# Kernel tuning notes

Measured on AMD Instinct MI355X. Metric: run time of the kernel, lower is better.

## Reference

```python
import jax, jax.numpy as jnp
import numpy as np

B, T, N = 32, 1024, 256
D = 1024          # latent_dim
TD = 768          # text_latent_dim
H = 16            # num_head
C = D // H        # head dim
TE = 2048         # time_embed_dim
EPS = 1e-5


def layer_norm(x, g, b):
    mu = jnp.mean(x, axis=-1, keepdims=True)
    var = jnp.var(x, axis=-1, keepdims=True)
    return (x - mu) * jax.lax.rsqrt(var + EPS) * g + b


def setup_inputs() -> dict:
    key = jax.random.key(0)
    ks = jax.random.split(key, 16)
    s_d = 1.0 / np.sqrt(D)
    s_td = 1.0 / np.sqrt(TD)
    s_te = 1.0 / np.sqrt(TE)
    return {
        "x": jax.random.normal(ks[0], (B, T, D), jnp.float32),
        "xf": jax.random.normal(ks[1], (B, N, TD), jnp.float32),
        "emb": jax.random.normal(ks[2], (B, TE), jnp.float32),
        "norm_g": jnp.ones((D,), jnp.float32),
        "norm_b": jnp.zeros((D,), jnp.float32),
        "tnorm_g": jnp.ones((TD,), jnp.float32),
        "tnorm_b": jnp.zeros((TD,), jnp.float32),
        "Wq": jax.random.normal(ks[3], (D, D), jnp.float32) * s_d,
        "bq": jnp.zeros((D,), jnp.float32),
        "Wk": jax.random.normal(ks[4], (TD, D), jnp.float32) * s_td,
        "bk": jnp.zeros((D,), jnp.float32),
        "Wv": jax.random.normal(ks[5], (TD, D), jnp.float32) * s_td,
        "bv": jnp.zeros((D,), jnp.float32),
        "emb_W": jax.random.normal(ks[6], (TE, 2 * D), jnp.float32) * s_te,
        "emb_b": jnp.zeros((2 * D,), jnp.float32),
        "fnorm_g": jnp.ones((D,), jnp.float32),
        "fnorm_b": jnp.zeros((D,), jnp.float32),
        "out_W": jax.random.normal(ks[7], (D, D), jnp.float32) * s_d,
        "out_b": jnp.zeros((D,), jnp.float32),
    }


def reference(x, xf, emb, norm_g, norm_b, tnorm_g, tnorm_b, Wq, bq, Wk, bk, Wv, bv,
              emb_W, emb_b, fnorm_g, fnorm_b, out_W, out_b):
    # projections from normalized inputs
    xn = layer_norm(x, norm_g, norm_b)            # [B,T,D]
    xfn = layer_norm(xf, tnorm_g, tnorm_b)        # [B,N,TD]
    q = (xn @ Wq + bq).reshape(B, T, H, C)        # [B,T,H,C]
    k = (xfn @ Wk + bk).reshape(B, N, H, C)       # [B,N,H,C]
    v = (xfn @ Wv + bv).reshape(B, N, H, C)       # [B,N,H,C]
    # dual softmax: query over channel dim, key over sequence dim
    q = jax.nn.softmax(q, axis=-1)
    k = jax.nn.softmax(k, axis=1)
    # linear attention: attn = k^T v over sequence, then q @ attn
    attn = jnp.einsum('bnhc,bnhd->bhcd', k, v)    # [B,H,C,C]
    y = jnp.einsum('bthc,bhcd->bthd', q, attn).reshape(B, T, D)
    # FiLM / StylizationBlock (dropout = identity at eval)
    e = jax.nn.silu(emb) @ emb_W + emb_b          # [B,2D]
    scale, shift = jnp.split(e[:, None, :], 2, axis=2)
    h = layer_norm(y, fnorm_g, fnorm_b) * (1.0 + scale) + shift
    h = jax.nn.silu(h) @ out_W + out_b
    return x + h
```

## Files before the change

kernel.cpp:

```cpp
#include <hip/hip_runtime.h>
#include <hip/hip_bf16.h>
#include <stdint.h>

#define B_  32
#define T_  1024
#define N_  256
#define D_  1024
#define TD_ 768
#define H_  16
#define C_  64
#define TE_ 2048

typedef __bf16 bf16x8 __attribute__((ext_vector_type(8)));
typedef __bf16 bf16x4 __attribute__((ext_vector_type(4)));
typedef float  f32x4  __attribute__((ext_vector_type(4)));

__device__ __forceinline__ void gll16(const void* g, void* l) {
  __builtin_amdgcn_global_load_lds(
      (const __attribute__((address_space(1))) unsigned int*)g,
      (__attribute__((address_space(3))) unsigned int*)l, 16, 0, 0);
}

__global__ void fill_val(float* o, float v, int n) {
  int i = blockIdx.x * 256 + threadIdx.x;
  if (i < n) o[i] = v;
}

__global__ void concat2(const float* __restrict__ a, const float* __restrict__ b,
                        float* __restrict__ o) {
  int i = blockIdx.x * 256 + threadIdx.x;
  if (i < 1024) o[i] = a[i];
  else if (i < 2048) o[i] = b[i - 1024];
}

__global__ void transpose_cast(const float* __restrict__ in,
                               __bf16* __restrict__ out, int R, int C) {
  __shared__ float t[32][33];
  int c0 = blockIdx.x * 32, r0 = blockIdx.y * 32;
  int x = threadIdx.x, y4 = threadIdx.y;
#pragma unroll
  for (int i = 0; i < 4; i++) {
    int rr = y4 * 4 + i;
    t[rr][x] = in[(size_t)(r0 + rr) * C + c0 + x];
  }
  __syncthreads();
#pragma unroll
  for (int i = 0; i < 4; i++) {
    int rr = y4 * 4 + i;
    out[(size_t)(c0 + rr) * R + r0 + x] = (__bf16)t[x][rr];
  }
}

__global__ __launch_bounds__(256)
void ln1024(const float* __restrict__ x, const float* __restrict__ g,
            const float* __restrict__ bb, __bf16* __restrict__ out) {
  size_t row = blockIdx.x;
  int c4 = threadIdx.x * 4;
  f32x4 v = *(const f32x4*)(x + row * D_ + c4);
  float s = v[0] + v[1] + v[2] + v[3];
  float s2 = v[0]*v[0] + v[1]*v[1] + v[2]*v[2] + v[3]*v[3];
#pragma unroll
  for (int off = 32; off; off >>= 1) {
    s += __shfl_down(s, off);
    s2 += __shfl_down(s2, off);
  }
  __shared__ float red[8];
  int wave = threadIdx.x >> 6, lane = threadIdx.x & 63;
  if (lane == 0) { red[wave] = s; red[4 + wave] = s2; }
  __syncthreads();
  if (threadIdx.x == 0) {
    float a = 0.f, c = 0.f;
    for (int w = 0; w < 4; w++) { a += red[w]; c += red[4 + w]; }
    red[0] = a; red[4] = c;
  }
  __syncthreads();
  float mu = red[0] / D_;
  float var = red[4] / D_ - mu * mu;
  float rstd = rsqrtf(var + 1e-5f);
  f32x4 gg = *(const f32x4*)(g + c4);
  f32x4 bbv = *(const f32x4*)(bb + c4);
  bf16x4 o;
#pragma unroll
  for (int t = 0; t < 4; t++) o[t] = (__bf16)((v[t] - mu) * rstd * gg[t] + bbv[t]);
  *(bf16x4*)(out + row * D_ + c4) = o;
}

__global__ __launch_bounds__(256)
void ln_rows(const float* __restrict__ x, const float* __restrict__ g,
             const float* __restrict__ bb, __bf16* __restrict__ out, int D) {
  size_t row = blockIdx.x;
  const float* xr = x + row * (size_t)D;
  int tid = threadIdx.x;
  int cnt = D >> 8;
  float v[4];
  float s = 0.f, s2 = 0.f;
  for (int i = 0; i < cnt; i++) {
    float f = xr[tid + i * 256];
    v[i] = f; s += f; s2 += f * f;
  }
#pragma unroll
  for (int off = 32; off; off >>= 1) {
    s += __shfl_down(s, off);
    s2 += __shfl_down(s2, off);
  }
  __shared__ float red[8];
  int wave = tid >> 6, lane = tid & 63;
  if (lane == 0) { red[wave] = s; red[4 + wave] = s2; }
  __syncthreads();
  if (tid == 0) {
    float a = 0.f, c = 0.f;
    for (int w = 0; w < 4; w++) { a += red[w]; c += red[4 + w]; }
    red[0] = a; red[4] = c;
  }
  __syncthreads();
  float mu = red[0] / D;
  float var = red[4] / D - mu * mu;
  float rstd = rsqrtf(var + 1e-5f);
  for (int i = 0; i < cnt; i++) {
    int c = tid + i * 256;
    out[row * (size_t)D + c] = (__bf16)((v[i] - mu) * rstd * g[c] + bb[c]);
  }
}

#define WB_(n) asm volatile("s_waitcnt vmcnt(" #n ")" ::: "memory")
#define WB(n) WB_(n)
#define BARR() asm volatile("s_barrier" ::: "memory")
#define LGKM0()                                             \
  do {                                                      \
    asm volatile("s_waitcnt lgkmcnt(0)" ::: "memory");      \
    __builtin_amdgcn_sched_barrier(0);                      \
  } while (0)

template <int EPI, typename CT>
__global__ __launch_bounds__(512, 2)
void gemm256(const __bf16* __restrict__ A, const __bf16* __restrict__ BT,
             const float* __restrict__ bias, const float* __restrict__ res,
             CT* __restrict__ C, int M, int N, int K, int NT) {
  __shared__ char smem[131072];
  const int tid = threadIdx.x;
  const int ln = tid & 63, wv = tid >> 6;

  const int nwg = gridDim.x;
  const int swz = (blockIdx.x & 7) * (nwg >> 3) + (blockIdx.x >> 3);
  const int m0 = (swz / NT) * 256, n0 = (swz % NT) * 256;

  const int wm = (wv >> 2) * 128, wn = (wv & 3) * 64;
  const int lr = ln & 15;
  const int xorv = (lr & 7) << 4;
  const int k16 = (ln >> 4) * 16;
  const int koff0 = k16 ^ xorv;
  const int koff1 = (64 + k16) ^ xorv;

  const int brow = tid >> 3;
  const int bseg = (tid & 7) ^ (brow & 7);
  const __bf16* Bg = BT + (size_t)(n0 + brow) * K + bseg * 8;
  const int ahalf = tid >> 8, au = tid & 255;
  const int arow = au >> 3;
  const int aseg = (au & 7) ^ (arow & 7);
  const __bf16* Ag = A + (size_t)(m0 + ahalf * 128 + arow) * K + aseg * 8;

  char* sBstage = smem + wv * 1024;
  char* sAstage = smem + 32768 + ahalf * 16384 + (wv & 3) * 1024;

  const int nt = K >> 6;
  f32x4 acc[8][4] = {};
  bf16x8 bfr[4][2], af[2][2];

#define STAGE_B(bf, s, k0) \
  gll16(Bg + (size_t)(s) * 64 * K + (k0), sBstage + (bf) * 65536 + (s) * 8192)
#define STAGE_A(bf, p, k0) \
  gll16(Ag + (size_t)(p) * 32 * K + (k0), sAstage + (bf) * 65536 + (p) * 4096)
#define LDA(pp, ar, kf) \
  (*(const bf16x8*)(sArd + ((wm + (pp) * 32 + (ar) * 16 + lr) * 128) + (kf)))

#define DO_MFMA(pp)                                                          \
  do {                                                                       \
    __builtin_amdgcn_s_setprio(1);                                           \
    _Pragma("unroll") for (int ar = 0; ar < 2; ++ar) {                       \
      _Pragma("unroll") for (int j = 0; j < 4; ++j) {                        \
        acc[(pp) * 2 + ar][j] = __builtin_amdgcn_mfma_f32_16x16x32_bf16(     \
            af[ar][0], bfr[j][0], acc[(pp) * 2 + ar][j], 0, 0, 0);           \
        acc[(pp) * 2 + ar][j] = __builtin_amdgcn_mfma_f32_16x16x32_bf16(     \
            af[ar][1], bfr[j][1], acc[(pp) * 2 + ar][j], 0, 0, 0);           \
      }                                                                      \
    }                                                                        \
    __builtin_amdgcn_s_setprio(0);                                           \
    __builtin_amdgcn_sched_barrier(0);                                       \
  } while (0)

#define TILE(buf, kst, PF, e0, e1, e2, e3)                                   \
  do {                                                                       \
    const char* sBrd = smem + (buf) * 65536;                                 \
    const char* sArd = sBrd + 32768;                                         \
                                                \
    if (PF) { STAGE_B((buf) ^ 1, 0, kst); STAGE_B((buf) ^ 1, 1, kst); }      \
    _Pragma("unroll") for (int j = 0; j < 4; ++j) {                          \
      bfr[j][0] = *(const bf16x8*)(sBrd + (wn + j * 16 + lr) * 128 + koff0); \
      bfr[j][1] = *(const bf16x8*)(sBrd + (wn + j * 16 + lr) * 128 + koff1); \
    }                                                                        \
    af[0][0] = LDA(0, 0, koff0); af[0][1] = LDA(0, 0, koff1);                \
    af[1][0] = LDA(0, 1, koff0); af[1][1] = LDA(0, 1, koff1);                \
    BARR(); LGKM0();                                                         \
    DO_MFMA(0);                                                              \
    WB(e0); BARR();                                                          \
                                                \
    if (PF) { STAGE_B((buf) ^ 1, 2, kst); STAGE_B((buf) ^ 1, 3, kst); }      \
    af[0][0] = LDA(1, 0, koff0); af[0][1] = LDA(1, 0, koff1);                \
    af[1][0] = LDA(1, 1, koff0); af[1][1] = LDA(1, 1, koff1);                \
    BARR(); LGKM0();                                                         \
    DO_MFMA(1);                                                              \
    WB(e1); BARR();                                                          \
                                                \
    if (PF) { STAGE_A((buf) ^ 1, 0, kst); STAGE_A((buf) ^ 1, 1, kst); }      \
    af[0][0] = LDA(2, 0, koff0); af[0][1] = LDA(2, 0, koff1);                \
    af[1][0] = LDA(2, 1, koff0); af[1][1] = LDA(2, 1, koff1);                \
    BARR(); LGKM0();                                                         \
    DO_MFMA(2);                                                              \
    WB(e2); BARR();                                                          \
                                                \
    if (PF) { STAGE_A((buf) ^ 1, 2, kst); STAGE_A((buf) ^ 1, 3, kst); }      \
    af[0][0] = LDA(3, 0, koff0); af[0][1] = LDA(3, 0, koff1);                \
    af[1][0] = LDA(3, 1, koff0); af[1][1] = LDA(3, 1, koff1);                \
    BARR(); LGKM0();                                                         \
    DO_MFMA(3);                                                              \
    WB(e3); BARR();                                                          \
  } while (0)

  STAGE_B(0, 0, 0); STAGE_B(0, 1, 0); STAGE_B(0, 2, 0); STAGE_B(0, 3, 0);
  STAGE_A(0, 0, 0); STAGE_A(0, 1, 0); STAGE_A(0, 2, 0); STAGE_A(0, 3, 0);
  WB(3); BARR();

  int kst = 64;
  const int npair = (nt >> 1) - 1;
  for (int tt = 0; tt < npair; ++tt) {
    TILE(0, kst, 1, 4, 5, 6, 3); kst += 64;
    TILE(1, kst, 1, 4, 5, 6, 3); kst += 64;
  }
  TILE(0, kst, 1, 4, 5, 6, 3);
  TILE(1, 0, 0, 2, 1, 0, 0);

#undef TILE
#undef DO_MFMA
#undef LDA
#undef STAGE_A
#undef STAGE_B

  __syncthreads();
  float* scratch = (float*)smem + wv * 1088;
  const int qd = ln >> 4;
#pragma unroll
  for (int i = 0; i < 8; ++i) {
#pragma unroll
    for (int j = 0; j < 4; ++j)
#pragma unroll
      for (int r = 0; r < 4; ++r)
        scratch[(qd * 4 + r) * 68 + j * 16 + lr] = acc[i][j][r];
    asm volatile("s_waitcnt lgkmcnt(0)" ::: "memory");
#pragma unroll
    for (int s = 0; s < 4; ++s) {
      int rr = qd + 4 * s;
      f32x4 vv = *(f32x4*)&scratch[rr * 68 + lr * 4];
      int row = m0 + wm + i * 16 + rr;
      int col = n0 + wn + lr * 4;
      size_t idx = (size_t)row * N + col;
      vv += *(const f32x4*)&bias[col];
      if (EPI == 1) vv += *(const f32x4*)&res[idx];
      if constexpr (sizeof(CT) == 4) {
        *(f32x4*)&C[idx] = vv;
      } else {
        bf16x4 o;
#pragma unroll
        for (int t2 = 0; t2 < 4; ++t2) o[t2] = (__bf16)vv[t2];
        *(bf16x4*)&C[idx] = o;
      }
    }
    asm volatile("s_waitcnt lgkmcnt(0)" ::: "memory");
  }
}

__global__ __launch_bounds__(256)
void kv_attn(const __bf16* __restrict__ kv, float* __restrict__ attn) {
  int h = blockIdx.x & 15, b = blockIdx.x >> 4;
  __shared__ __bf16 sK[256 * 72];
  __shared__ float sV[32 * 64];
  __shared__ float sInv[64];
  int tid = threadIdx.x;
  const __bf16* kb = kv + (size_t)b * N_ * 2048 + h * C_;
  const __bf16* vb = kb + 1024;

  {
    const __bf16* src = kb + (size_t)tid * 2048;
#pragma unroll
    for (int j = 0; j < 8; j++)
      *(bf16x8*)&sK[tid * 72 + j * 8] = *(const bf16x8*)(src + j * 8);
  }
  __syncthreads();

  {
    int c = tid >> 2, qq = tid & 3;
    float m = -1e30f;
    for (int t = 0; t < 64; t++)
      m = fmaxf(m, (float)sK[(qq * 64 + t) * 72 + c]);
    m = fmaxf(m, __shfl_xor(m, 1));
    m = fmaxf(m, __shfl_xor(m, 2));
    float s = 0.f;
    for (int t = 0; t < 64; t++) {
      int idx = (qq * 64 + t) * 72 + c;
      float e = __expf((float)sK[idx] - m);
      sK[idx] = (__bf16)e;
      s += e;
    }
    s += __shfl_xor(s, 1);
    s += __shfl_xor(s, 2);
    if (qq == 0) sInv[c] = 1.f / s;
  }
  __syncthreads();

  int c0 = (tid & 15) * 4, d0 = (tid >> 4) * 4;
  float acc[4][4] = {};
  for (int n0 = 0; n0 < N_; n0 += 32) {
    __syncthreads();
    {
      int r = tid >> 3, s8 = (tid & 7) * 8;
      bf16x8 vv8 = *(const bf16x8*)(vb + (size_t)(n0 + r) * 2048 + s8);
#pragma unroll
      for (int j = 0; j < 8; j++) sV[r * 64 + s8 + j] = (float)vv8[j];
    }
    __syncthreads();
    for (int n = 0; n < 32; n++) {
      bf16x4 kk = *(const bf16x4*)&sK[(n0 + n) * 72 + c0];
      f32x4 vd = *(const f32x4*)&sV[n * 64 + d0];
#pragma unroll
      for (int i = 0; i < 4; i++) {
        float kf = (float)kk[i];
#pragma unroll
        for (int j = 0; j < 4; j++) acc[i][j] += kf * vd[j];
      }
    }
  }
  float* ab = attn + (size_t)(b * H_ + h) * 4096;
#pragma unroll
  for (int i = 0; i < 4; i++) {
    float inv = sInv[c0 + i];
    f32x4 o;
#pragma unroll
    for (int j = 0; j < 4; j++) o[j] = acc[i][j] * inv;
    *(f32x4*)&ab[(c0 + i) * 64 + d0] = o;
  }
}

__global__ __launch_bounds__(256)
void qattn_y(const __bf16* __restrict__ q, const float* __restrict__ attn,
             __bf16* __restrict__ y) {
  int tt = blockIdx.x * 64;
  int h = blockIdx.y, b = blockIdx.z;
  __shared__ float sQ[64 * 65];
  __shared__ float sA[64 * 64];
  int tid = threadIdx.x;
  const __bf16* qb = q + ((size_t)b * T_ + tt) * D_ + h * C_;
#pragma unroll
  for (int it = 0; it < 2; it++) {
    int r = (tid >> 3) + it * 32;
    int cc = (tid & 7) * 8;
    bf16x8 vv = *(const bf16x8*)(qb + (size_t)r * D_ + cc);
#pragma unroll
    for (int j = 0; j < 8; j++) sQ[(cc + j) * 65 + r] = (float)vv[j];
  }
  const float* ab = attn + (size_t)(b * H_ + h) * 4096;
  for (int i = tid; i < 1024; i += 256) ((f32x4*)sA)[i] = ((const f32x4*)ab)[i];
  __syncthreads();
  {
    int r = tid >> 2, sub = tid & 3;
    float m = -1e30f;
#pragma unroll
    for (int j = 0; j < 16; j++)
      m = fmaxf(m, sQ[(sub * 16 + j) * 65 + r]);
    m = fmaxf(m, __shfl_xor(m, 1));
    m = fmaxf(m, __shfl_xor(m, 2));
    float s = 0.f;
#pragma unroll
    for (int j = 0; j < 16; j++) {
      int idx = (sub * 16 + j) * 65 + r;
      float e = __expf(sQ[idx] - m);
      sQ[idx] = e;
      s += e;
    }
    s += __shfl_xor(s, 1);
    s += __shfl_xor(s, 2);
    float inv = 1.f / s;
#pragma unroll
    for (int j = 0; j < 16; j++) sQ[(sub * 16 + j) * 65 + r] *= inv;
  }
  __syncthreads();
  int r0 = (tid >> 4) * 4, d0 = (tid & 15) * 4;
  float acc[4][4] = {};
  for (int c = 0; c < 64; c++) {
    f32x4 qv = *(const f32x4*)&sQ[c * 65 + r0];
    f32x4 av = *(const f32x4*)&sA[c * 64 + d0];
#pragma unroll
    for (int i = 0; i < 4; i++)
#pragma unroll
      for (int j = 0; j < 4; j++) acc[i][j] += qv[i] * av[j];
  }
  __bf16* yb = y + ((size_t)b * T_ + tt) * D_ + h * C_;
#pragma unroll
  for (int i = 0; i < 4; i++) {
    bf16x4 o;
#pragma unroll
    for (int j = 0; j < 4; j++) o[j] = (__bf16)acc[i][j];
    *(bf16x4*)(yb + (size_t)(r0 + i) * D_ + d0) = o;
  }
}

__global__ __launch_bounds__(256)
void emb_gemm(const float* __restrict__ emb, const float* __restrict__ W,
              const float* __restrict__ eb, float* __restrict__ ss) {
  int b = blockIdx.x >> 3;
  int n = (blockIdx.x & 7) * 256 + threadIdx.x;
  __shared__ float se[TE_];
  for (int i = threadIdx.x; i < TE_; i += 256) {
    float xv = emb[(size_t)b * TE_ + i];
    se[i] = xv / (1.f + __expf(-xv));
  }
  __syncthreads();
  float acc = 0.f;
  for (int kk = 0; kk < TE_; kk++) acc += se[kk] * W[(size_t)kk * 2048 + n];
  ss[(size_t)b * 2048 + n] = acc + eb[n];
}

__global__ __launch_bounds__(256)
void film_rows(const __bf16* __restrict__ y, const float* __restrict__ ss,
               const float* __restrict__ g, const float* __restrict__ bb,
               __bf16* __restrict__ out) {
  size_t row = blockIdx.x;
  int b = (int)(row >> 10);
  int c4 = threadIdx.x * 4;
  bf16x4 yv = *(const bf16x4*)(y + row * D_ + c4);
  float v[4];
  float s = 0.f, s2 = 0.f;
#pragma unroll
  for (int t = 0; t < 4; t++) {
    v[t] = (float)yv[t];
    s += v[t]; s2 += v[t] * v[t];
  }
#pragma unroll
  for (int off = 32; off; off >>= 1) {
    s += __shfl_down(s, off);
    s2 += __shfl_down(s2, off);
  }
  __shared__ float red[8];
  int wave = threadIdx.x >> 6, lane = threadIdx.x & 63;
  if (lane == 0) { red[wave] = s; red[4 + wave] = s2; }
  __syncthreads();
  if (threadIdx.x == 0) {
    float a = 0.f, c = 0.f;
    for (int w = 0; w < 4; w++) { a += red[w]; c += red[4 + w]; }
    red[0] = a; red[4] = c;
  }
  __syncthreads();
  float mu = red[0] / D_;
  float var = red[4] / D_ - mu * mu;
  float rstd = rsqrtf(var + 1e-5f);
  f32x4 gg = *(const f32x4*)(g + c4);
  f32x4 bbv = *(const f32x4*)(bb + c4);
  f32x4 sc = *(const f32x4*)(ss + (size_t)b * 2048 + c4);
  f32x4 sh = *(const f32x4*)(ss + (size_t)b * 2048 + 1024 + c4);
  bf16x4 o;
#pragma unroll
  for (int t = 0; t < 4; t++) {
    float ln = (v[t] - mu) * rstd * gg[t] + bbv[t];
    float hh = ln * (1.f + sc[t]) + sh[t];
    o[t] = (__bf16)(hh / (1.f + __expf(-hh)));
  }
  *(bf16x4*)(out + row * D_ + c4) = o;
}

extern "C" void kernel_launch(void* const* d_in, const int* in_sizes, int n_in,
                              void* d_out, int out_size, void* d_ws,
                              size_t ws_size, hipStream_t stream) {
  (void)in_sizes; (void)n_in;
  const float* x       = (const float*)d_in[0];
  const float* xf      = (const float*)d_in[1];
  const float* emb     = (const float*)d_in[2];
  const float* norm_g  = (const float*)d_in[3];
  const float* norm_b  = (const float*)d_in[4];
  const float* tnorm_g = (const float*)d_in[5];
  const float* tnorm_b = (const float*)d_in[6];
  const float* Wq      = (const float*)d_in[7];
  const float* bq      = (const float*)d_in[8];
  const float* Wk      = (const float*)d_in[9];
  const float* bk      = (const float*)d_in[10];
  const float* Wv      = (const float*)d_in[11];
  const float* bv      = (const float*)d_in[12];
  const float* emb_W   = (const float*)d_in[13];
  const float* emb_b   = (const float*)d_in[14];
  const float* fnorm_g = (const float*)d_in[15];
  const float* fnorm_b = (const float*)d_in[16];
  const float* out_W   = (const float*)d_in[17];
  const float* out_b   = (const float*)d_in[18];
  float* out = (float*)d_out;

  const size_t SZ_WQT  = (size_t)D_ * D_ * 2;
  const size_t SZ_WKVT = (size_t)2048 * TD_ * 2;
  const size_t SZ_XN   = (size_t)B_ * T_ * D_ * 2;
  const size_t SZ_XFN  = (size_t)B_ * N_ * TD_ * 2;
  const size_t SZ_KV   = (size_t)B_ * N_ * 2048 * 2;
  const size_t SZ_BKV  = 2048 * 4;
  const size_t NEED = SZ_WQT * 2 + SZ_WKVT + SZ_XN + SZ_XFN + SZ_KV + SZ_BKV;

  if (ws_size < NEED) {
    fill_val<<<(out_size + 255) / 256, 256, 0, stream>>>(
        out, (float)(ws_size >> 20), out_size);
    return;
  }

  char* w = (char*)d_ws;
  __bf16* WqT  = (__bf16*)w; w += SZ_WQT;
  __bf16* WkvT = (__bf16*)w; w += SZ_WKVT;
  __bf16* WoT  = (__bf16*)w; w += SZ_WQT;
  __bf16* xn   = (__bf16*)w; w += SZ_XN;
  char*   xfnR = w;          w += SZ_XFN;
  __bf16* kvbuf= (__bf16*)w; w += SZ_KV;
  float*  bkv  = (float*)w;  w += SZ_BKV;
  __bf16* xfn  = (__bf16*)xfnR;
  float*  attn = (float*)xfnR;
  float*  ss   = (float*)(xfnR + (size_t)B_ * H_ * C_ * C_ * 4);
  __bf16* hpre = xn;
  __bf16* qbuf = (__bf16*)out;
  __bf16* ybuf = qbuf;

  transpose_cast<<<dim3(D_ / 32, D_ / 32), dim3(32, 8), 0, stream>>>(Wq, WqT, D_, D_);
  transpose_cast<<<dim3(D_ / 32, TD_ / 32), dim3(32, 8), 0, stream>>>(Wk, WkvT, TD_, D_);
  transpose_cast<<<dim3(D_ / 32, TD_ / 32), dim3(32, 8), 0, stream>>>(
      Wv, WkvT + (size_t)1024 * TD_, TD_, D_);
  transpose_cast<<<dim3(D_ / 32, D_ / 32), dim3(32, 8), 0, stream>>>(out_W, WoT, D_, D_);
  concat2<<<8, 256, 0, stream>>>(bk, bv, bkv);

  ln1024<<<B_ * T_, 256, 0, stream>>>(x, norm_g, norm_b, xn);
  ln_rows<<<B_ * N_, 256, 0, stream>>>(xf, tnorm_g, tnorm_b, xfn, TD_);

  gemm256<0, __bf16><<<dim3((B_ * T_ / 256) * (D_ / 256)), 512, 0, stream>>>(
      xn, WqT, bq, nullptr, qbuf, B_ * T_, D_, D_, D_ / 256);
  gemm256<0, __bf16><<<dim3((B_ * N_ / 256) * (2048 / 256)), 512, 0, stream>>>(
      xfn, WkvT, bkv, nullptr, kvbuf, B_ * N_, 2048, TD_, 2048 / 256);

  kv_attn<<<B_ * H_, 256, 0, stream>>>(kvbuf, attn);

  qattn_y<<<dim3(T_ / 64, H_, B_), 256, 0, stream>>>(qbuf, attn, ybuf);

  emb_gemm<<<B_ * 8, 256, 0, stream>>>(emb, emb_W, emb_b, ss);
  film_rows<<<B_ * T_, 256, 0, stream>>>(ybuf, ss, fnorm_g, fnorm_b, hpre);

  gemm256<1, float><<<dim3((B_ * T_ / 256) * (D_ / 256)), 512, 0, stream>>>(
      hpre, WoT, out_b, x, out, B_ * T_, D_, D_, D_ / 256);
}
```

Before: 741.3 us.

## Fuse weight prep launches, rebalance GEMM prefetch, split-K emb GEMM, widen kv tile

Merges the four weight transpose-casts and the bias concat into one prep_weights launch to cut launch overhead. The GEMM tile schedule now issues all B-stage prefetches in the first phase and spreads the A-stage loads across the later phases, with adjusted wait counts. The emb GEMM is split four ways along K, using atomicAdd onto a bias-initialized buffer to raise parallelism. kv_attn now processes 64 rows of V per sync instead of 32, halving the barriers. The atomics make the emb result order-dependent, and the new wait counts must match the reordered loads.

```diff
diff --git a/kernel.cpp b/kernel.cpp
--- a/kernel.cpp
+++ b/kernel.cpp
@@ -26,17 +26,11 @@
   if (i < n) o[i] = v;
 }
 
-__global__ void concat2(const float* __restrict__ a, const float* __restrict__ b,
-                        float* __restrict__ o) {
-  int i = blockIdx.x * 256 + threadIdx.x;
-  if (i < 1024) o[i] = a[i];
-  else if (i < 2048) o[i] = b[i - 1024];
-}
-
-__global__ void transpose_cast(const float* __restrict__ in,
-                               __bf16* __restrict__ out, int R, int C) {
+__device__ __forceinline__ void tc_block(const float* __restrict__ in,
+                                         __bf16* __restrict__ out, int R, int C,
+                                         int bx, int by) {
   __shared__ float t[32][33];
-  int c0 = blockIdx.x * 32, r0 = blockIdx.y * 32;
+  int c0 = bx * 32, r0 = by * 32;
   int x = threadIdx.x, y4 = threadIdx.y;
 #pragma unroll
   for (int i = 0; i < 4; i++) {
@@ -49,6 +43,31 @@
     int rr = y4 * 4 + i;
     out[(size_t)(c0 + rr) * R + r0 + x] = (__bf16)t[x][rr];
   }
+}
+
+__global__ void prep_weights(const float* __restrict__ Wq,
+                             const float* __restrict__ Wk,
+                             const float* __restrict__ Wv,
+                             const float* __restrict__ Wo,
+                             const float* __restrict__ bk,
+                             const float* __restrict__ bv,
+                             __bf16* __restrict__ WqT, __bf16* __restrict__ WkvT,
+                             __bf16* __restrict__ WoT, float* __restrict__ bkv) {
+  int bid = blockIdx.x;
+  if (bid < 1024) { tc_block(Wq, WqT, D_, D_, bid & 31, bid >> 5); return; }
+  bid -= 1024;
+  if (bid < 768) { tc_block(Wk, WkvT, TD_, D_, bid & 31, bid >> 5); return; }
+  bid -= 768;
+  if (bid < 768) {
+    tc_block(Wv, WkvT + (size_t)1024 * TD_, TD_, D_, bid & 31, bid >> 5);
+    return;
+  }
+  bid -= 768;
+  if (bid < 1024) { tc_block(Wo, WoT, D_, D_, bid & 31, bid >> 5); return; }
+  bid -= 1024;
+  int i = bid * 256 + threadIdx.y * 32 + threadIdx.x;
+  if (i < 1024) bkv[i] = bk[i];
+  else if (i < 2048) bkv[i] = bv[i - 1024];
 }
 
 __global__ __launch_bounds__(256)
@@ -192,8 +211,11 @@
   do {                                                                       \
     const char* sBrd = smem + (buf) * 65536;                                 \
     const char* sArd = sBrd + 32768;                                         \
-                                                \
-    if (PF) { STAGE_B((buf) ^ 1, 0, kst); STAGE_B((buf) ^ 1, 1, kst); }      \
+                                      \
+    if (PF) {                                                                \
+      STAGE_B((buf) ^ 1, 0, kst); STAGE_B((buf) ^ 1, 1, kst);                \
+      STAGE_B((buf) ^ 1, 2, kst); STAGE_B((buf) ^ 1, 3, kst);                \
+    }                                                                        \
     _Pragma("unroll") for (int j = 0; j < 4; ++j) {                          \
       bfr[j][0] = *(const bf16x8*)(sBrd + (wn + j * 16 + lr) * 128 + koff0); \
       bfr[j][1] = *(const bf16x8*)(sBrd + (wn + j * 16 + lr) * 128 + koff1); \
@@ -203,22 +225,22 @@
     BARR(); LGKM0();                                                         \
     DO_MFMA(0);                                                              \
     WB(e0); BARR();                                                          \
-                                                \
-    if (PF) { STAGE_B((buf) ^ 1, 2, kst); STAGE_B((buf) ^ 1, 3, kst); }      \
+                                                 \
+    if (PF) { STAGE_A((buf) ^ 1, 0, kst); }                                  \
     af[0][0] = LDA(1, 0, koff0); af[0][1] = LDA(1, 0, koff1);                \
     af[1][0] = LDA(1, 1, koff0); af[1][1] = LDA(1, 1, koff1);                \
     BARR(); LGKM0();                                                         \
     DO_MFMA(1);                                                              \
     WB(e1); BARR();                                                          \
-                                                \
-    if (PF) { STAGE_A((buf) ^ 1, 0, kst); STAGE_A((buf) ^ 1, 1, kst); }      \
+                                              \
+    if (PF) { STAGE_A((buf) ^ 1, 1, kst); STAGE_A((buf) ^ 1, 2, kst); }      \
     af[0][0] = LDA(2, 0, koff0); af[0][1] = LDA(2, 0, koff1);                \
     af[1][0] = LDA(2, 1, koff0); af[1][1] = LDA(2, 1, koff1);                \
     BARR(); LGKM0();                                                         \
     DO_MFMA(2);                                                              \
     WB(e2); BARR();                                                          \
-                                                \
-    if (PF) { STAGE_A((buf) ^ 1, 2, kst); STAGE_A((buf) ^ 1, 3, kst); }      \
+                                                 \
+    if (PF) { STAGE_A((buf) ^ 1, 3, kst); }                                  \
     af[0][0] = LDA(3, 0, koff0); af[0][1] = LDA(3, 0, koff1);                \
     af[1][0] = LDA(3, 1, koff0); af[1][1] = LDA(3, 1, koff1);                \
     BARR(); LGKM0();                                                         \
@@ -233,10 +255,10 @@
   int kst = 64;
   const int npair = (nt >> 1) - 1;
   for (int tt = 0; tt < npair; ++tt) {
-    TILE(0, kst, 1, 4, 5, 6, 3); kst += 64;
-    TILE(1, kst, 1, 4, 5, 6, 3); kst += 64;
-  }
-  TILE(0, kst, 1, 4, 5, 6, 3);
+    TILE(0, kst, 1, 6, 6, 7, 3); kst += 64;
+    TILE(1, kst, 1, 6, 6, 7, 3); kst += 64;
+  }
+  TILE(0, kst, 1, 6, 6, 7, 3);
   TILE(1, 0, 0, 2, 1, 0, 0);
 
 #undef TILE
@@ -282,7 +304,7 @@
 void kv_attn(const __bf16* __restrict__ kv, float* __restrict__ attn) {
   int h = blockIdx.x & 15, b = blockIdx.x >> 4;
   __shared__ __bf16 sK[256 * 72];
-  __shared__ float sV[32 * 64];
+  __shared__ float sV[64 * 64];
   __shared__ float sInv[64];
   int tid = threadIdx.x;
   const __bf16* kb = kv + (size_t)b * N_ * 2048 + h * C_;
@@ -318,16 +340,21 @@
 
   int c0 = (tid & 15) * 4, d0 = (tid >> 4) * 4;
   float acc[4][4] = {};
-  for (int n0 = 0; n0 < N_; n0 += 32) {
+  for (int n0 = 0; n0 < N_; n0 += 64) {
     __syncthreads();
     {
-      int r = tid >> 3, s8 = (tid & 7) * 8;
-      bf16x8 vv8 = *(const bf16x8*)(vb + (size_t)(n0 + r) * 2048 + s8);
-#pragma unroll
-      for (int j = 0; j < 8; j++) sV[r * 64 + s8 + j] = (float)vv8[j];
+      int r = tid >> 2, s8 = (tid & 3) * 16;
+      const __bf16* vr = vb + (size_t)(n0 + r) * 2048 + s8;
+      bf16x8 a0 = *(const bf16x8*)vr;
+      bf16x8 a1 = *(const bf16x8*)(vr + 8);
+#pragma unroll
+      for (int j = 0; j < 8; j++) {
+        sV[r * 64 + s8 + j] = (float)a0[j];
+        sV[r * 64 + s8 + 8 + j] = (float)a1[j];
+      }
     }
     __syncthreads();
-    for (int n = 0; n < 32; n++) {
+    for (int n = 0; n < 64; n++) {
       bf16x4 kk = *(const bf16x4*)&sK[(n0 + n) * 72 + c0];
       f32x4 vd = *(const f32x4*)&sV[n * 64 + d0];
 #pragma unroll
@@ -413,19 +440,28 @@
 }
 
 __global__ __launch_bounds__(256)
+void ss_init(const float* __restrict__ eb, float* __restrict__ ss) {
+  int i = blockIdx.x * 256 + threadIdx.x;
+  ss[i] = eb[i & 2047];
+}
+
+__global__ __launch_bounds__(256)
 void emb_gemm(const float* __restrict__ emb, const float* __restrict__ W,
-              const float* __restrict__ eb, float* __restrict__ ss) {
-  int b = blockIdx.x >> 3;
-  int n = (blockIdx.x & 7) * 256 + threadIdx.x;
-  __shared__ float se[TE_];
-  for (int i = threadIdx.x; i < TE_; i += 256) {
-    float xv = emb[(size_t)b * TE_ + i];
+              float* __restrict__ ss) {
+  int b  = blockIdx.x >> 5;
+  int nc = (blockIdx.x >> 2) & 7;
+  int kq = blockIdx.x & 3;
+  __shared__ float se[512];
+  int k0 = kq * 512;
+  for (int i = threadIdx.x; i < 512; i += 256) {
+    float xv = emb[(size_t)b * TE_ + k0 + i];
     se[i] = xv / (1.f + __expf(-xv));
   }
   __syncthreads();
+  int n = nc * 256 + threadIdx.x;
   float acc = 0.f;
-  for (int kk = 0; kk < TE_; kk++) acc += se[kk] * W[(size_t)kk * 2048 + n];
-  ss[(size_t)b * 2048 + n] = acc + eb[n];
+  for (int kk = 0; kk < 512; kk++) acc += se[kk] * W[(size_t)(k0 + kk) * 2048 + n];
+  atomicAdd(&ss[(size_t)b * 2048 + n], acc);
 }
 
 __global__ __launch_bounds__(256)
@@ -529,12 +565,8 @@
   __bf16* qbuf = (__bf16*)out;
   __bf16* ybuf = qbuf;
 
-  transpose_cast<<<dim3(D_ / 32, D_ / 32), dim3(32, 8), 0, stream>>>(Wq, WqT, D_, D_);
-  transpose_cast<<<dim3(D_ / 32, TD_ / 32), dim3(32, 8), 0, stream>>>(Wk, WkvT, TD_, D_);
-  transpose_cast<<<dim3(D_ / 32, TD_ / 32), dim3(32, 8), 0, stream>>>(
-      Wv, WkvT + (size_t)1024 * TD_, TD_, D_);
-  transpose_cast<<<dim3(D_ / 32, D_ / 32), dim3(32, 8), 0, stream>>>(out_W, WoT, D_, D_);
-  concat2<<<8, 256, 0, stream>>>(bk, bv, bkv);
+  prep_weights<<<3592, dim3(32, 8), 0, stream>>>(Wq, Wk, Wv, out_W, bk, bv,
+                                                 WqT, WkvT, WoT, bkv);
 
   ln1024<<<B_ * T_, 256, 0, stream>>>(x, norm_g, norm_b, xn);
   ln_rows<<<B_ * N_, 256, 0, stream>>>(xf, tnorm_g, tnorm_b, xfn, TD_);
@@ -548,7 +580,8 @@
 
   qattn_y<<<dim3(T_ / 64, H_, B_), 256, 0, stream>>>(qbuf, attn, ybuf);
 
-  emb_gemm<<<B_ * 8, 256, 0, stream>>>(emb, emb_W, emb_b, ss);
+  ss_init<<<256, 256, 0, stream>>>(emb_b, ss);
+  emb_gemm<<<B_ * 32, 256, 0, stream>>>(emb, emb_W, ss);
   film_rows<<<B_ * T_, 256, 0, stream>>>(ybuf, ss, fnorm_g, fnorm_b, hpre);
 
   gemm256<1, float><<<dim3((B_ * T_ / 256) * (D_ / 256)), 512, 0, stream>>>(
```

New measurement: 661.4 us. 10.8% less time.
